# Kernel tuning notes

Hardware: AMD Instinct MI355X
Metric: run time of the kernel (lower is better)

## Reference

```python
import jax, jax.numpy as jnp
import numpy as np

KERNEL_SIZE = 7


def setup_inputs() -> dict:
    key = jax.random.key(0)
    x = jax.random.normal(key, (32, 4096, 512), dtype=jnp.float32)  # [B, L, C]
    return {"x": x, "dilation": 1}


def reference(x, dilation):
    """Box-filter (mean) conv1d, kernel 7, circular padding, applied per channel.
    x: [B, L, C] -> [B, L, C]
    Fused as a single depthwise conv instead of a Python loop over C.
    """
    B, L, C = x.shape
    pad = dilation * (KERNEL_SIZE - 1) // 2
    xt = jnp.transpose(x, (0, 2, 1))  # [B, C, L]
    # circular padding, matching padding_mode='circular'
    xp = jnp.pad(xt, ((0, 0), (0, 0), (pad, pad)), mode="wrap")  # [B, C, L+2*pad]
    # uniform box-filter weights 1/7, one per channel (depthwise)
    w = jnp.full((C, 1, KERNEL_SIZE), 1.0 / KERNEL_SIZE, dtype=x.dtype)  # [C, 1, K]
    y = jax.lax.conv_general_dilated(
        xp, w,
        window_strides=(1,),
        padding="VALID",
        rhs_dilation=(dilation,),
        dimension_numbers=("NCH", "OIH", "NCH"),
        feature_group_count=C,
    )  # [B, C, L]
    return jnp.transpose(y, (0, 2, 1))  # [B, L, C]
```

## Files before the change

kernel.cpp:

```cpp
#include <hip/hip_runtime.h>


typedef float f32x4 __attribute__((ext_vector_type(4)));

constexpr int Bv = 32;
constexpr int Lv = 4096;
constexpr int Cv = 512;
constexpr int C4 = Cv / 4;
constexpr int T  = 32;
constexpr int STRIPS = Lv / T;
constexpr int NBLOCKS = Bv * STRIPS * C4 / 256;
constexpr int NXCD = 8;
constexpr int CHUNK = NBLOCKS / NXCD;

__global__ __launch_bounds__(256) void box7_kernel(const f32x4* __restrict__ x,
                                                   f32x4* __restrict__ y) {
    const int blk = (blockIdx.x & (NXCD - 1)) * CHUNK + (blockIdx.x >> 3);
    const int tid = blk * 256 + threadIdx.x;

    const int c4 = tid & (C4 - 1);
    const int s  = (tid >> 7) & (STRIPS - 1);
    const int b  = tid >> 14;

    const int l0 = s * T;
    const size_t base = (size_t)b * Lv * C4 + (size_t)c4;

    f32x4 w[7];
#pragma unroll
    for (int i = 0; i < 7; ++i) {
        int li = l0 - 3 + i;
        li = (li < 0) ? (li + Lv) : ((li >= Lv) ? (li - Lv) : li);
        w[i] = x[base + (size_t)li * C4];
    }

    const float inv7 = 1.0f / 7.0f;

#pragma unroll
    for (int t = 0; t < T; ++t) {
        f32x4 o;
        o.x = (((w[0].x + w[1].x) + (w[2].x + w[3].x)) + ((w[4].x + w[5].x) + w[6].x)) * inv7;
        o.y = (((w[0].y + w[1].y) + (w[2].y + w[3].y)) + ((w[4].y + w[5].y) + w[6].y)) * inv7;
        o.z = (((w[0].z + w[1].z) + (w[2].z + w[3].z)) + ((w[4].z + w[5].z) + w[6].z)) * inv7;
        o.w = (((w[0].w + w[1].w) + (w[2].w + w[3].w)) + ((w[4].w + w[5].w) + w[6].w)) * inv7;

        __builtin_nontemporal_store(o, &y[base + (size_t)(l0 + t) * C4]);

        if (t < T - 1) {
            int li = l0 + t + 4;
            if (li >= Lv) li -= Lv;
            w[t % 7] = x[base + (size_t)li * C4];
        }
    }
}

extern "C" void kernel_launch(void* const* d_in, const int* in_sizes, int n_in,
                              void* d_out, int out_size, void* d_ws, size_t ws_size,
                              hipStream_t stream) {
    const f32x4* x = (const f32x4*)d_in[0];
    f32x4* y = (f32x4*)d_out;

    box7_kernel<<<NBLOCKS, 256, 0, stream>>>(x, y);
}
```

Before: 459.1 us.

## Map one wavefront per row strip covering both channel halves, halve strip length

```diff
diff --git a/kernel.cpp b/kernel.cpp
--- a/kernel.cpp
+++ b/kernel.cpp
@@ -7,48 +7,66 @@
 constexpr int Lv = 4096;
 constexpr int Cv = 512;
 constexpr int C4 = Cv / 4;
-constexpr int T  = 32;
+constexpr int T  = 16;
 constexpr int STRIPS = Lv / T;
-constexpr int NBLOCKS = Bv * STRIPS * C4 / 256;
-constexpr int NXCD = 8;
-constexpr int CHUNK = NBLOCKS / NXCD;
+constexpr int NWAVES = Bv * STRIPS;
+constexpr int NBLOCKS = NWAVES / 4;
 
 __global__ __launch_bounds__(256) void box7_kernel(const f32x4* __restrict__ x,
                                                    f32x4* __restrict__ y) {
-    const int blk = (blockIdx.x & (NXCD - 1)) * CHUNK + (blockIdx.x >> 3);
-    const int tid = blk * 256 + threadIdx.x;
-
-    const int c4 = tid & (C4 - 1);
-    const int s  = (tid >> 7) & (STRIPS - 1);
-    const int b  = tid >> 14;
+    const int tid  = blockIdx.x * 256 + threadIdx.x;
+    const int lane = tid & 63;
+    const int wid  = tid >> 6;
+    const int s    = wid & (STRIPS - 1);
+    const int b    = wid >> 8;
 
     const int l0 = s * T;
-    const size_t base = (size_t)b * Lv * C4 + (size_t)c4;
+    const size_t rowbase = (size_t)b * Lv * C4;
+    const int cA = lane;
+    const int cB = lane + 64;
 
-    f32x4 w[7];
+    f32x4 wA[7], wB[7];
 #pragma unroll
     for (int i = 0; i < 7; ++i) {
         int li = l0 - 3 + i;
         li = (li < 0) ? (li + Lv) : ((li >= Lv) ? (li - Lv) : li);
-        w[i] = x[base + (size_t)li * C4];
+        const f32x4* row = x + rowbase + (size_t)li * C4;
+        wA[i] = row[cA];
+        wB[i] = row[cB];
     }
 
     const float inv7 = 1.0f / 7.0f;
 
 #pragma unroll
     for (int t = 0; t < T; ++t) {
-        f32x4 o;
-        o.x = (((w[0].x + w[1].x) + (w[2].x + w[3].x)) + ((w[4].x + w[5].x) + w[6].x)) * inv7;
-        o.y = (((w[0].y + w[1].y) + (w[2].y + w[3].y)) + ((w[4].y + w[5].y) + w[6].y)) * inv7;
-        o.z = (((w[0].z + w[1].z) + (w[2].z + w[3].z)) + ((w[4].z + w[5].z) + w[6].z)) * inv7;
-        o.w = (((w[0].w + w[1].w) + (w[2].w + w[3].w)) + ((w[4].w + w[5].w) + w[6].w)) * inv7;
+        const f32x4 a0 = wA[(t + 0) % 7], b0 = wB[(t + 0) % 7];
+        const f32x4 a1 = wA[(t + 1) % 7], b1 = wB[(t + 1) % 7];
+        const f32x4 a2 = wA[(t + 2) % 7], b2 = wB[(t + 2) % 7];
+        const f32x4 a3 = wA[(t + 3) % 7], b3 = wB[(t + 3) % 7];
+        const f32x4 a4 = wA[(t + 4) % 7], b4 = wB[(t + 4) % 7];
+        const f32x4 a5 = wA[(t + 5) % 7], b5 = wB[(t + 5) % 7];
+        const f32x4 a6 = wA[(t + 6) % 7], b6 = wB[(t + 6) % 7];
 
-        __builtin_nontemporal_store(o, &y[base + (size_t)(l0 + t) * C4]);
+        f32x4 oA, oB;
+        oA.x = (((a0.x + a1.x) + (a2.x + a3.x)) + ((a4.x + a5.x) + a6.x)) * inv7;
+        oA.y = (((a0.y + a1.y) + (a2.y + a3.y)) + ((a4.y + a5.y) + a6.y)) * inv7;
+        oA.z = (((a0.z + a1.z) + (a2.z + a3.z)) + ((a4.z + a5.z) + a6.z)) * inv7;
+        oA.w = (((a0.w + a1.w) + (a2.w + a3.w)) + ((a4.w + a5.w) + a6.w)) * inv7;
+        oB.x = (((b0.x + b1.x) + (b2.x + b3.x)) + ((b4.x + b5.x) + b6.x)) * inv7;
+        oB.y = (((b0.y + b1.y) + (b2.y + b3.y)) + ((b4.y + b5.y) + b6.y)) * inv7;
+        oB.z = (((b0.z + b1.z) + (b2.z + b3.z)) + ((b4.z + b5.z) + b6.z)) * inv7;
+        oB.w = (((b0.w + b1.w) + (b2.w + b3.w)) + ((b4.w + b5.w) + b6.w)) * inv7;
+
+        f32x4* yrow = y + rowbase + (size_t)(l0 + t) * C4;
+        yrow[cA] = oA;
+        yrow[cB] = oB;
 
         if (t < T - 1) {
             int li = l0 + t + 4;
             if (li >= Lv) li -= Lv;
-            w[t % 7] = x[base + (size_t)li * C4];
+            const f32x4* row = x + rowbase + (size_t)li * C4;
+            wA[t % 7] = row[cA];
+            wB[t % 7] = row[cB];
         }
     }
 }
```

Measured after the change: 440.7 us. -4.0%, faster.
